# Kernel optimization log

Hardware: AMD Instinct MI355X
Metric: run time of the kernel (lower is better)

The kernel has to match this reference:

```python
import jax, jax.numpy as jnp
import numpy as np

B, V, K = 128, 128000, 20
_SAMPLING_EPS = 1e-5


def setup_inputs() -> dict:
    key = jax.random.key(0)
    k1, k2, k3 = jax.random.split(key, 3)
    logits = jax.random.normal(k1, (B, V), dtype=jnp.float32)
    temp = jax.random.uniform(k2, (B,), dtype=jnp.float32, minval=0.2, maxval=1.5)
    # every 4th sequence is greedy (temperature < eps)
    temp = jnp.where(jnp.arange(B) % 4 == 0, 0.0, temp)
    # uniform noise in (0,1); exponential noise is q = -log(u)
    u = jax.random.uniform(k3, (B, V), dtype=jnp.float32, minval=1e-7, maxval=1.0)
    return {"logits": logits, "temp": temp, "u": u, "max_num_logprobs": K}


def reference(logits, temp, u, max_num_logprobs):
    # apply_temperature: greedy rows (temp < eps) use temp=1.0
    t = jnp.where(temp < _SAMPLING_EPS, 1.0, temp)
    scaled = logits.astype(jnp.float32) / t[:, None]          # [B, V]
    probs = jax.nn.softmax(scaled, axis=-1)                    # [B, V]
    # greedy sample
    greedy = jnp.argmax(probs, axis=1)                         # [B]
    # random sample via exponential-race (Gumbel-max equivalent): argmax(probs / Exp(1))
    q = -jnp.log(u)                                            # Exp(1) noise
    random_sampled = jnp.argmax(probs / q, axis=1)             # [B]
    sampled = jnp.where(temp < _SAMPLING_EPS, greedy, random_sampled)
    # top-k logprobs
    logprobs = jax.nn.log_softmax(scaled, axis=-1)             # [B, V]
    topk_logprobs, topk_indices = jax.lax.top_k(logprobs, max_num_logprobs)
    return sampled, topk_logprobs, topk_indices
```

## Files before the change

kernel.cpp:

```cpp
#include <hip/hip_runtime.h>
#include <stdint.h>


#define KMAX 20
#define SAMPLING_EPS 1e-5f
#define TAU 3.0f
#define CPB 64
#define LOG2E 1.44269504f
#define SMARGIN 3e-4f

static __device__ __forceinline__ float fexp2(float x) {
#if __has_builtin(__builtin_amdgcn_exp2f)
    return __builtin_amdgcn_exp2f(x);
#else
    return exp2f(x);
#endif
}

static __device__ __forceinline__ unsigned int ord32(float v) {
    unsigned int u = __float_as_uint(v);
    return u ^ ((unsigned int)((int)u >> 31) | 0x80000000u);
}
static __device__ __forceinline__ float unord32(unsigned int x) {
    unsigned int u = (x & 0x80000000u) ? (x ^ 0x80000000u) : ~x;
    return __uint_as_float(u);
}
static __device__ __forceinline__ unsigned long long shflxor64(unsigned long long v, int off) {
    int lo = __shfl_xor((int)(unsigned int)v, off, 64);
    int hi = __shfl_xor((int)(unsigned int)(v >> 32), off, 64);
    return ((unsigned long long)(unsigned int)hi << 32) | (unsigned int)lo;
}

static __device__ __forceinline__ float gumbel_exact(float x, float inv_t, float uu, float wm) {
    const float q = (uu > 0.984375f) ? -log1pf(-wm) : -__logf(uu);
    return x * inv_t - __logf(q);
}

static __device__ __forceinline__ float gub_bound(float a, float uu) {
    return fmaf((float)__float_as_uint(1.0f - uu), -0x1p-23f, 127.0f + a);
}

__global__ __launch_bounds__(256, 6) void k1_partials(
        const float* __restrict__ logits, const float* __restrict__ u,
        const float* __restrict__ temp,
        unsigned int* __restrict__ wrec,
        unsigned int* __restrict__ cntbuf,
        uint2* __restrict__ candbuf,
        int V, int nsplit) {
    __shared__ int cnt;
    __shared__ uint2 cand[CPB];
    const int b = blockIdx.x;
    const int t = threadIdx.x;
    const int lane = t & 63;
    const int w = t >> 6;
    if (t == 0) cnt = 0;
    __syncthreads();

    const int nrows = gridDim.x / nsplit;
    const int mb = b % nrows;
    const int sp = b / nrows;
    int r = (mb * 61 + (sp >> 1)) % nrows;
    if ((nrows & (nrows - 1)) == 0) r ^= (r >> 4);
    const int slot = r * nsplit + sp;

    const float traw = temp[r];
    const bool greedy = traw < SAMPLING_EPS;
    const float inv_t = greedy ? 1.0f : (1.0f / traw);
    const float it2 = inv_t * LOG2E;

    const int nf4 = V >> 2;
    const int per = (nf4 + nsplit - 1) / nsplit;
    const int f0 = sp * per;
    const int f1 = min(f0 + per, nf4);

    const float4* __restrict__ l4 = (const float4*)(logits + (size_t)r * V);
    const float4* __restrict__ u4 = (const float4*)(u + (size_t)r * V);

    float s0 = 0.0f, s1 = 0.0f, s2 = 0.0f, s3 = 0.0f;
    float gv = -INFINITY;
    int gcol = 0;

#define PUSH(xv, cc) do { \
        const int pi_ = atomicAdd(&cnt, 1); \
        if (pi_ < CPB) cand[pi_] = make_uint2(__float_as_uint(xv), (unsigned)(cc)); \
    } while (0)

    if (greedy) {
        int f = f0 + t;
        for (; f + 256 < f1; f += 512) {
            const float4 la = l4[f];
            const float4 lb = l4[f + 256];
            s0 += fexp2(la.x * it2); s1 += fexp2(la.y * it2);
            s2 += fexp2(la.z * it2); s3 += fexp2(la.w * it2);
            s0 += fexp2(lb.x * it2); s1 += fexp2(lb.y * it2);
            s2 += fexp2(lb.z * it2); s3 += fexp2(lb.w * it2);
            const float xm = fmaxf(fmaxf(fmaxf(la.x, la.y), fmaxf(la.z, la.w)),
                                   fmaxf(fmaxf(lb.x, lb.y), fmaxf(lb.z, lb.w)));
            if (xm >= TAU) {
                const int c0 = f << 2, c1 = (f + 256) << 2;
                if (la.x >= TAU) PUSH(la.x, c0);
                if (la.y >= TAU) PUSH(la.y, c0 + 1);
                if (la.z >= TAU) PUSH(la.z, c0 + 2);
                if (la.w >= TAU) PUSH(la.w, c0 + 3);
                if (lb.x >= TAU) PUSH(lb.x, c1);
                if (lb.y >= TAU) PUSH(lb.y, c1 + 1);
                if (lb.z >= TAU) PUSH(lb.z, c1 + 2);
                if (lb.w >= TAU) PUSH(lb.w, c1 + 3);
            }
        }
        for (; f < f1; f += 256) {
            const float4 la = l4[f];
            s0 += fexp2(la.x * it2); s1 += fexp2(la.y * it2);
            s2 += fexp2(la.z * it2); s3 += fexp2(la.w * it2);
            const float xm = fmaxf(fmaxf(la.x, la.y), fmaxf(la.z, la.w));
            if (xm >= TAU) {
                const int c0 = f << 2;
                if (la.x >= TAU) PUSH(la.x, c0);
                if (la.y >= TAU) PUSH(la.y, c0 + 1);
                if (la.z >= TAU) PUSH(la.z, c0 + 2);
                if (la.w >= TAU) PUSH(la.w, c0 + 3);
            }
        }
    } else {
        int f = f0 + t;
        if (f < f1) {
            const float4 la = l4[f];
            const float4 ua = u4[f];
            const int c0 = f << 2;
            s0 += fexp2(la.x * it2); s1 += fexp2(la.y * it2);
            s2 += fexp2(la.z * it2); s3 += fexp2(la.w * it2);
            { const float g = gumbel_exact(la.x, inv_t, ua.x, 1.0f - ua.x);
              if (g > gv) { gv = g; gcol = c0; } }
            { const float g = gumbel_exact(la.y, inv_t, ua.y, 1.0f - ua.y);
              if (g > gv) { gv = g; gcol = c0 + 1; } }
            { const float g = gumbel_exact(la.z, inv_t, ua.z, 1.0f - ua.z);
              if (g > gv) { gv = g; gcol = c0 + 2; } }
            { const float g = gumbel_exact(la.w, inv_t, ua.w, 1.0f - ua.w);
              if (g > gv) { gv = g; gcol = c0 + 3; } }
            const float xm = fmaxf(fmaxf(la.x, la.y), fmaxf(la.z, la.w));
            if (xm >= TAU) {
                if (la.x >= TAU) PUSH(la.x, c0);
                if (la.y >= TAU) PUSH(la.y, c0 + 1);
                if (la.z >= TAU) PUSH(la.z, c0 + 2);
                if (la.w >= TAU) PUSH(la.w, c0 + 3);
            }
        }
        float gmax = gv;
        #pragma unroll
        for (int off = 1; off < 64; off <<= 1) gmax = fmaxf(gmax, __shfl_xor(gmax, off, 64));
        float gvs2 = fmaf(gmax, LOG2E, -SMARGIN);

#define EX(gj, xv, uu, cc) \
        if ((gj) > gvs2) { \
            const float wm_ = 1.0f - (uu); \
            const float ge_ = gumbel_exact(xv, inv_t, uu, wm_); \
            if (ge_ > gv) { gv = ge_; gcol = (cc); gvs2 = fmaf(ge_, LOG2E, -SMARGIN); } \
        }

        for (f += 256; f + 256 < f1; f += 512) {
            const float4 la = l4[f];
            const float4 lb = l4[f + 256];
            const float4 ua = u4[f];
            const float4 ub = u4[f + 256];
            const float a0 = la.x * it2, a1 = la.y * it2, a2 = la.z * it2, a3 = la.w * it2;
            const float a4 = lb.x * it2, a5 = lb.y * it2, a6 = lb.z * it2, a7 = lb.w * it2;
            s0 += fexp2(a0); s1 += fexp2(a1); s2 += fexp2(a2); s3 += fexp2(a3);
            s0 += fexp2(a4); s1 += fexp2(a5); s2 += fexp2(a6); s3 += fexp2(a7);
            const float g0 = gub_bound(a0, ua.x), g1 = gub_bound(a1, ua.y);
            const float g2 = gub_bound(a2, ua.z), g3 = gub_bound(a3, ua.w);
            const float g4 = gub_bound(a4, ub.x), g5 = gub_bound(a5, ub.y);
            const float g6 = gub_bound(a6, ub.z), g7 = gub_bound(a7, ub.w);
            const float gm = fmaxf(fmaxf(fmaxf(g0, g1), fmaxf(g2, g3)),
                                   fmaxf(fmaxf(g4, g5), fmaxf(g6, g7)));
            if (gm > gvs2) {
                const int c0 = f << 2, c1 = (f + 256) << 2;
                EX(g0, la.x, ua.x, c0)
                EX(g1, la.y, ua.y, c0 + 1)
                EX(g2, la.z, ua.z, c0 + 2)
                EX(g3, la.w, ua.w, c0 + 3)
                EX(g4, lb.x, ub.x, c1)
                EX(g5, lb.y, ub.y, c1 + 1)
                EX(g6, lb.z, ub.z, c1 + 2)
                EX(g7, lb.w, ub.w, c1 + 3)
            }
            const float xm = fmaxf(fmaxf(fmaxf(la.x, la.y), fmaxf(la.z, la.w)),
                                   fmaxf(fmaxf(lb.x, lb.y), fmaxf(lb.z, lb.w)));
            if (xm >= TAU) {
                const int c0 = f << 2, c1 = (f + 256) << 2;
                if (la.x >= TAU) PUSH(la.x, c0);
                if (la.y >= TAU) PUSH(la.y, c0 + 1);
                if (la.z >= TAU) PUSH(la.z, c0 + 2);
                if (la.w >= TAU) PUSH(la.w, c0 + 3);
                if (lb.x >= TAU) PUSH(lb.x, c1);
                if (lb.y >= TAU) PUSH(lb.y, c1 + 1);
                if (lb.z >= TAU) PUSH(lb.z, c1 + 2);
                if (lb.w >= TAU) PUSH(lb.w, c1 + 3);
            }
        }
        for (; f < f1; f += 256) {
            const float4 la = l4[f];
            const float4 ua = u4[f];
            const float a0 = la.x * it2, a1 = la.y * it2, a2 = la.z * it2, a3 = la.w * it2;
            s0 += fexp2(a0); s1 += fexp2(a1); s2 += fexp2(a2); s3 += fexp2(a3);
            const float g0 = gub_bound(a0, ua.x), g1 = gub_bound(a1, ua.y);
            const float g2 = gub_bound(a2, ua.z), g3 = gub_bound(a3, ua.w);
            const float gm = fmaxf(fmaxf(g0, g1), fmaxf(g2, g3));
            if (gm > gvs2) {
                const int c0 = f << 2;
                EX(g0, la.x, ua.x, c0)
                EX(g1, la.y, ua.y, c0 + 1)
                EX(g2, la.z, ua.z, c0 + 2)
                EX(g3, la.w, ua.w, c0 + 3)
            }
            const float xm = fmaxf(fmaxf(la.x, la.y), fmaxf(la.z, la.w));
            if (xm >= TAU) {
                const int c0 = f << 2;
                if (la.x >= TAU) PUSH(la.x, c0);
                if (la.y >= TAU) PUSH(la.y, c0 + 1);
                if (la.z >= TAU) PUSH(la.z, c0 + 2);
                if (la.w >= TAU) PUSH(la.w, c0 + 3);
            }
        }
#undef EX
    }
#undef PUSH

    float s = (s0 + s1) + (s2 + s3);
    #pragma unroll
    for (int off = 1; off < 64; off <<= 1) s += __shfl_xor(s, off, 64);
    unsigned long long gk = greedy ? 0ull
        : (((unsigned long long)ord32(gv) << 32) | (unsigned int)~(unsigned int)gcol);
    #pragma unroll
    for (int off = 1; off < 64; off <<= 1) {
        const unsigned long long o = shflxor64(gk, off);
        gk = (o > gk) ? o : gk;
    }
    if (lane == 0) {
        unsigned int* rp = wrec + (size_t)(slot * 4 + w) * 4;
        rp[0] = __float_as_uint(s);
        rp[1] = __float_as_uint(unord32((unsigned int)(gk >> 32)));
        rp[2] = ~(unsigned int)gk;
    }
    __syncthreads();
    const int c = cnt;
    if (t == 0) cntbuf[slot] = (unsigned)c;
    if (t < min(c, CPB)) candbuf[(size_t)slot * CPB + t] = cand[t];
}

__global__ __launch_bounds__(64) void k2_finalize(
        const unsigned int* __restrict__ wrec, const unsigned int* __restrict__ cntbuf,
        const uint2* __restrict__ candbuf, const float* __restrict__ logits,
        const float* __restrict__ temp, float* __restrict__ out,
        int B, int V, int K, int nsplit) {
    __shared__ unsigned long long kbuf[512];
    const int r = blockIdx.x;
    const int lane = threadIdx.x;
    const int NW = nsplit * 4;

    const float traw = temp[r];
    const bool greedy = traw < SAMPLING_EPS;
    const float tt = greedy ? 1.0f : traw;

    float s = 0.0f;
    unsigned long long gk = 0ull;
    if (lane < NW) {
        const unsigned int* rp = wrec + (size_t)(r * NW + lane) * 4;
        s = __uint_as_float(rp[0]);
        gk = ((unsigned long long)ord32(__uint_as_float(rp[1])) << 32) | (unsigned int)~rp[2];
    }
    #pragma unroll
    for (int off = 1; off < 64; off <<= 1) s += __shfl_xor(s, off, 64);
    #pragma unroll
    for (int off = 1; off < 64; off <<= 1) {
        const unsigned long long o = shflxor64(gk, off);
        gk = (o > gk) ? o : gk;
    }
    const float lS = logf(s);

    const int cnt_raw = (lane < nsplit) ? (int)cntbuf[r * nsplit + lane] : 0;
    const int cntc = min(cnt_raw, CPB);
    const bool ovf = __ballot(cnt_raw > CPB) != 0ull;
    int incl = cntc;
    #pragma unroll
    for (int d = 1; d < 64; d <<= 1) {
        const int o = __shfl_up(incl, d, 64);
        if (lane >= d) incl += o;
    }
    const int T = __shfl(incl, 63, 64);
    const int off0 = incl - cntc;

    unsigned long long keys[8];
    #pragma unroll
    for (int jj = 0; jj < 8; ++jj) keys[jj] = 0ull;

    if (!ovf && T >= K && T <= 512) {
        if (lane < nsplit) {
            const uint2* cb = candbuf + (size_t)(r * nsplit + lane) * CPB;
            for (int i = 0; i < cntc; ++i) {
                const uint2 e = cb[i];
                kbuf[off0 + i] = ((unsigned long long)ord32(__uint_as_float(e.x)) << 32)
                               | (unsigned int)~e.y;
            }
        }
        __syncthreads();
        #pragma unroll
        for (int jj = 0; jj < 8; ++jj) {
            const int idx = lane + 64 * jj;
            if (idx < T) keys[jj] = kbuf[idx];
        }
    } else {
        unsigned long long mykey = ((unsigned long long)0x007FFFFFu) << 32;
        unsigned long long minkey = mykey;
        float vmin = -INFINITY;
        const float* lr = logits + (size_t)r * V;
        for (int base = 0; base < V; base += 64) {
            const int i = base + lane;
            const float x = (i < V) ? lr[i] : -INFINITY;
            unsigned long long cm = __ballot((i < V) && (x >= vmin));
            while (cm) {
                const int src = (int)__builtin_ctzll(cm);
                cm &= cm - 1;
                const float cv = __shfl(x, src, 64);
                const int cc = __shfl(i, src, 64);
                const unsigned long long ck =
                    ((unsigned long long)ord32(cv) << 32) | (unsigned int)~(unsigned int)cc;
                if (ck > minkey) {
                    const bool own = (lane < K) && (mykey == minkey);
                    const unsigned long long om = __ballot(own);
                    if (lane == (int)__builtin_ctzll(om)) mykey = ck;
                    unsigned long long mk = (lane < K) ? mykey : ~0ull;
                    #pragma unroll
                    for (int o2 = 1; o2 < 64; o2 <<= 1) {
                        const unsigned long long o = shflxor64(mk, o2);
                        mk = (o < mk) ? o : mk;
                    }
                    minkey = mk;
                    vmin = unord32((unsigned int)(mk >> 32));
                }
            }
        }
        keys[0] = (lane < K) ? mykey : 0ull;
    }

    float* out_s  = out;
    float* out_lp = out + B;
    float* out_ix = out + B + (size_t)B * K;

    unsigned int top1 = 0;
    for (int k = 0; k < K; ++k) {
        unsigned long long loc = keys[0];
        #pragma unroll
        for (int jj = 1; jj < 8; ++jj) loc = (keys[jj] > loc) ? keys[jj] : loc;
        #pragma unroll
        for (int off = 1; off < 64; off <<= 1) {
            const unsigned long long o = shflxor64(loc, off);
            loc = (o > loc) ? o : loc;
        }
        #pragma unroll
        for (int jj = 0; jj < 8; ++jj) if (keys[jj] == loc) keys[jj] = 0ull;
        if (lane == 0) {
            const unsigned int col = ~(unsigned int)loc;
            const float v = unord32((unsigned int)(loc >> 32));
            out_lp[(size_t)r * K + k] = v / tt - lS;
            out_ix[(size_t)r * K + k] = (float)col;
            if (k == 0) top1 = col;
        }
    }
    if (lane == 0) {
        out_s[r] = (float)(greedy ? top1 : (~(unsigned int)gk));
    }
}

extern "C" void kernel_launch(void* const* d_in, const int* in_sizes, int n_in,
                              void* d_out, int out_size, void* d_ws, size_t ws_size,
                              hipStream_t stream) {
    const float* logits = (const float*)d_in[0];
    const float* temp   = (const float*)d_in[1];
    const float* u      = (const float*)d_in[2];
    const int B = in_sizes[1];
    const int V = in_sizes[0] / B;
    int K = (out_size - B) / (2 * B);
    if (K > KMAX) K = KMAX;
    if (K < 1) K = 1;

    int nsplit = 16;
    while (nsplit > 1 && (size_t)B * nsplit * 580 > ws_size) nsplit >>= 1;
    const int blocks = B * nsplit;

    unsigned int* wrec   = (unsigned int*)d_ws;
    unsigned int* cntbuf = wrec + (size_t)blocks * 16;
    uint2*        candbf = (uint2*)(cntbuf + blocks);

    k1_partials<<<dim3(blocks), dim3(256), 0, stream>>>(
        logits, u, temp, wrec, cntbuf, candbf, V, nsplit);
    k2_finalize<<<dim3(B), dim3(64), 0, stream>>>(
        wrec, cntbuf, candbf, logits, temp, (float*)d_out, B, V, K, nsplit);
}
```

Baseline: 159.7 us.

## Stage logits and noise through LDS with async global_load_lds double buffering

Replaces the direct register-based float4 streaming loop with a tiled pipeline that copies logits and uniform noise into shared memory using the global_load_lds builtin. It keeps two tiles in flight and syncs twice per tile. Occupancy hint is raised from 6 to 8 waves per SIMD. The aim is to hide memory latency with asynchronous loads. In exchange it adds LDS traffic, two block barriers per 256-element tile, and drops the previous 2x unrolling.

```diff
diff --git a/kernel.cpp b/kernel.cpp
--- a/kernel.cpp
+++ b/kernel.cpp
@@ -8,6 +8,7 @@
 #define CPB 64
 #define LOG2E 1.44269504f
 #define SMARGIN 3e-4f
+#define TILE 256
 
 static __device__ __forceinline__ float fexp2(float x) {
 #if __has_builtin(__builtin_amdgcn_exp2f)
@@ -40,13 +41,25 @@
     return fmaf((float)__float_as_uint(1.0f - uu), -0x1p-23f, 127.0f + a);
 }
 
-__global__ __launch_bounds__(256, 6) void k1_partials(
+static __device__ __forceinline__ void g2lds(const float4* gaddr, float4* lds_wave_base, int lane) {
+#if __has_builtin(__builtin_amdgcn_global_load_lds)
+    __builtin_amdgcn_global_load_lds(
+        (const __attribute__((address_space(1))) void*)gaddr,
+        (__attribute__((address_space(3))) void*)lds_wave_base, 16, 0, 0);
+#else
+    lds_wave_base[lane] = *gaddr;
+#endif
+}
+
+__global__ __launch_bounds__(256, 8) void k1_partials(
         const float* __restrict__ logits, const float* __restrict__ u,
         const float* __restrict__ temp,
         unsigned int* __restrict__ wrec,
         unsigned int* __restrict__ cntbuf,
         uint2* __restrict__ candbuf,
         int V, int nsplit) {
+    __shared__ float4 sL[2][TILE];
+    __shared__ float4 sU[2][TILE];
     __shared__ int cnt;
     __shared__ uint2 cand[CPB];
     const int b = blockIdx.x;
@@ -54,7 +67,6 @@
     const int lane = t & 63;
     const int w = t >> 6;
     if (t == 0) cnt = 0;
-    __syncthreads();
 
     const int nrows = gridDim.x / nsplit;
     const int mb = b % nrows;
@@ -72,6 +84,8 @@
     const int per = (nf4 + nsplit - 1) / nsplit;
     const int f0 = sp * per;
     const int f1 = min(f0 + per, nf4);
+    const int len = f1 - f0;
+    const int ntiles = (len + TILE - 1) / TILE;
 
     const float4* __restrict__ l4 = (const float4*)(logits + (size_t)r * V);
     const float4* __restrict__ u4 = (const float4*)(u + (size_t)r * V);
@@ -79,64 +93,95 @@
     float s0 = 0.0f, s1 = 0.0f, s2 = 0.0f, s3 = 0.0f;
     float gv = -INFINITY;
     int gcol = 0;
+    float gvs2 = INFINITY;
+    const float4 z4 = make_float4(0.f, 0.f, 0.f, 0.f);
+
+#define STAGE(bb, tt) do { \
+        const int si_ = f0 + (tt) * TILE + t; \
+        if (si_ < f1) { \
+            g2lds(l4 + si_, &sL[bb][w * 64], lane); \
+            if (!greedy) g2lds(u4 + si_, &sU[bb][w * 64], lane); \
+        } \
+    } while (0)
 
 #define PUSH(xv, cc) do { \
         const int pi_ = atomicAdd(&cnt, 1); \
         if (pi_ < CPB) cand[pi_] = make_uint2(__float_as_uint(xv), (unsigned)(cc)); \
     } while (0)
 
-    if (greedy) {
-        int f = f0 + t;
-        for (; f + 256 < f1; f += 512) {
-            const float4 la = l4[f];
-            const float4 lb = l4[f + 256];
-            s0 += fexp2(la.x * it2); s1 += fexp2(la.y * it2);
-            s2 += fexp2(la.z * it2); s3 += fexp2(la.w * it2);
-            s0 += fexp2(lb.x * it2); s1 += fexp2(lb.y * it2);
-            s2 += fexp2(lb.z * it2); s3 += fexp2(lb.w * it2);
-            const float xm = fmaxf(fmaxf(fmaxf(la.x, la.y), fmaxf(la.z, la.w)),
-                                   fmaxf(fmaxf(lb.x, lb.y), fmaxf(lb.z, lb.w)));
-            if (xm >= TAU) {
-                const int c0 = f << 2, c1 = (f + 256) << 2;
-                if (la.x >= TAU) PUSH(la.x, c0);
-                if (la.y >= TAU) PUSH(la.y, c0 + 1);
-                if (la.z >= TAU) PUSH(la.z, c0 + 2);
-                if (la.w >= TAU) PUSH(la.w, c0 + 3);
-                if (lb.x >= TAU) PUSH(lb.x, c1);
-                if (lb.y >= TAU) PUSH(lb.y, c1 + 1);
-                if (lb.z >= TAU) PUSH(lb.z, c1 + 2);
-                if (lb.w >= TAU) PUSH(lb.w, c1 + 3);
-            }
-        }
-        for (; f < f1; f += 256) {
-            const float4 la = l4[f];
-            s0 += fexp2(la.x * it2); s1 += fexp2(la.y * it2);
-            s2 += fexp2(la.z * it2); s3 += fexp2(la.w * it2);
-            const float xm = fmaxf(fmaxf(la.x, la.y), fmaxf(la.z, la.w));
-            if (xm >= TAU) {
-                const int c0 = f << 2;
-                if (la.x >= TAU) PUSH(la.x, c0);
-                if (la.y >= TAU) PUSH(la.y, c0 + 1);
-                if (la.z >= TAU) PUSH(la.z, c0 + 2);
-                if (la.w >= TAU) PUSH(la.w, c0 + 3);
-            }
-        }
-    } else {
-        int f = f0 + t;
-        if (f < f1) {
-            const float4 la = l4[f];
-            const float4 ua = u4[f];
-            const int c0 = f << 2;
-            s0 += fexp2(la.x * it2); s1 += fexp2(la.y * it2);
-            s2 += fexp2(la.z * it2); s3 += fexp2(la.w * it2);
-            { const float g = gumbel_exact(la.x, inv_t, ua.x, 1.0f - ua.x);
-              if (g > gv) { gv = g; gcol = c0; } }
-            { const float g = gumbel_exact(la.y, inv_t, ua.y, 1.0f - ua.y);
-              if (g > gv) { gv = g; gcol = c0 + 1; } }
-            { const float g = gumbel_exact(la.z, inv_t, ua.z, 1.0f - ua.z);
-              if (g > gv) { gv = g; gcol = c0 + 2; } }
-            { const float g = gumbel_exact(la.w, inv_t, ua.w, 1.0f - ua.w);
-              if (g > gv) { gv = g; gcol = c0 + 3; } }
+    STAGE(0, 0);
+    if (ntiles > 1) STAGE(1, 1);
+
+    for (int k = 0; k < ntiles; ++k) {
+        __syncthreads();
+        const int idx = f0 + k * TILE + t;
+        const bool act = idx < f1;
+        const int cur = k & 1;
+        float4 la = z4, ua = z4;
+        if (act) {
+            la = sL[cur][t];
+            if (!greedy) ua = sU[cur][t];
+        }
+        __syncthreads();
+        if (k + 2 < ntiles) STAGE(cur, k + 2);
+
+        if (greedy) {
+            if (act) {
+                s0 += fexp2(la.x * it2); s1 += fexp2(la.y * it2);
+                s2 += fexp2(la.z * it2); s3 += fexp2(la.w * it2);
+                const float xm = fmaxf(fmaxf(la.x, la.y), fmaxf(la.z, la.w));
+                if (xm >= TAU) {
+                    const int c0 = idx << 2;
+                    if (la.x >= TAU) PUSH(la.x, c0);
+                    if (la.y >= TAU) PUSH(la.y, c0 + 1);
+                    if (la.z >= TAU) PUSH(la.z, c0 + 2);
+                    if (la.w >= TAU) PUSH(la.w, c0 + 3);
+                }
+            }
+        } else if (k == 0) {
+            if (act) {
+                const int c0 = idx << 2;
+                s0 += fexp2(la.x * it2); s1 += fexp2(la.y * it2);
+                s2 += fexp2(la.z * it2); s3 += fexp2(la.w * it2);
+                { const float g = gumbel_exact(la.x, inv_t, ua.x, 1.0f - ua.x);
+                  if (g > gv) { gv = g; gcol = c0; } }
+                { const float g = gumbel_exact(la.y, inv_t, ua.y, 1.0f - ua.y);
+                  if (g > gv) { gv = g; gcol = c0 + 1; } }
+                { const float g = gumbel_exact(la.z, inv_t, ua.z, 1.0f - ua.z);
+                  if (g > gv) { gv = g; gcol = c0 + 2; } }
+                { const float g = gumbel_exact(la.w, inv_t, ua.w, 1.0f - ua.w);
+                  if (g > gv) { gv = g; gcol = c0 + 3; } }
+                const float xm = fmaxf(fmaxf(la.x, la.y), fmaxf(la.z, la.w));
+                if (xm >= TAU) {
+                    if (la.x >= TAU) PUSH(la.x, c0);
+                    if (la.y >= TAU) PUSH(la.y, c0 + 1);
+                    if (la.z >= TAU) PUSH(la.z, c0 + 2);
+                    if (la.w >= TAU) PUSH(la.w, c0 + 3);
+                }
+            }
+            float gmax = gv;
+            #pragma unroll
+            for (int off = 1; off < 64; off <<= 1) gmax = fmaxf(gmax, __shfl_xor(gmax, off, 64));
+            gvs2 = fmaf(gmax, LOG2E, -SMARGIN);
+        } else if (act) {
+#define EX(gj, xv, uu, cc) \
+            if ((gj) > gvs2) { \
+                const float wm_ = 1.0f - (uu); \
+                const float ge_ = gumbel_exact(xv, inv_t, uu, wm_); \
+                if (ge_ > gv) { gv = ge_; gcol = (cc); gvs2 = fmaf(ge_, LOG2E, -SMARGIN); } \
+            }
+            const int c0 = idx << 2;
+            const float a0 = la.x * it2, a1 = la.y * it2, a2 = la.z * it2, a3 = la.w * it2;
+            s0 += fexp2(a0); s1 += fexp2(a1); s2 += fexp2(a2); s3 += fexp2(a3);
+            const float g0 = gub_bound(a0, ua.x), g1 = gub_bound(a1, ua.y);
+            const float g2 = gub_bound(a2, ua.z), g3 = gub_bound(a3, ua.w);
+            const float gm = fmaxf(fmaxf(g0, g1), fmaxf(g2, g3));
+            if (gm > gvs2) {
+                EX(g0, la.x, ua.x, c0)
+                EX(g1, la.y, ua.y, c0 + 1)
+                EX(g2, la.z, ua.z, c0 + 2)
+                EX(g3, la.w, ua.w, c0 + 3)
+            }
             const float xm = fmaxf(fmaxf(la.x, la.y), fmaxf(la.z, la.w));
             if (xm >= TAU) {
                 if (la.x >= TAU) PUSH(la.x, c0);
@@ -144,86 +189,11 @@
                 if (la.z >= TAU) PUSH(la.z, c0 + 2);
                 if (la.w >= TAU) PUSH(la.w, c0 + 3);
             }
-        }
-        float gmax = gv;
-        #pragma unroll
-        for (int off = 1; off < 64; off <<= 1) gmax = fmaxf(gmax, __shfl_xor(gmax, off, 64));
-        float gvs2 = fmaf(gmax, LOG2E, -SMARGIN);
-
-#define EX(gj, xv, uu, cc) \
-        if ((gj) > gvs2) { \
-            const float wm_ = 1.0f - (uu); \
-            const float ge_ = gumbel_exact(xv, inv_t, uu, wm_); \
-            if (ge_ > gv) { gv = ge_; gcol = (cc); gvs2 = fmaf(ge_, LOG2E, -SMARGIN); } \
-        }
-
-        for (f += 256; f + 256 < f1; f += 512) {
-            const float4 la = l4[f];
-            const float4 lb = l4[f + 256];
-            const float4 ua = u4[f];
-            const float4 ub = u4[f + 256];
-            const float a0 = la.x * it2, a1 = la.y * it2, a2 = la.z * it2, a3 = la.w * it2;
-            const float a4 = lb.x * it2, a5 = lb.y * it2, a6 = lb.z * it2, a7 = lb.w * it2;
-            s0 += fexp2(a0); s1 += fexp2(a1); s2 += fexp2(a2); s3 += fexp2(a3);
-            s0 += fexp2(a4); s1 += fexp2(a5); s2 += fexp2(a6); s3 += fexp2(a7);
-            const float g0 = gub_bound(a0, ua.x), g1 = gub_bound(a1, ua.y);
-            const float g2 = gub_bound(a2, ua.z), g3 = gub_bound(a3, ua.w);
-            const float g4 = gub_bound(a4, ub.x), g5 = gub_bound(a5, ub.y);
-            const float g6 = gub_bound(a6, ub.z), g7 = gub_bound(a7, ub.w);
-            const float gm = fmaxf(fmaxf(fmaxf(g0, g1), fmaxf(g2, g3)),
-                                   fmaxf(fmaxf(g4, g5), fmaxf(g6, g7)));
-            if (gm > gvs2) {
-                const int c0 = f << 2, c1 = (f + 256) << 2;
-                EX(g0, la.x, ua.x, c0)
-                EX(g1, la.y, ua.y, c0 + 1)
-                EX(g2, la.z, ua.z, c0 + 2)
-                EX(g3, la.w, ua.w, c0 + 3)
-                EX(g4, lb.x, ub.x, c1)
-                EX(g5, lb.y, ub.y, c1 + 1)
-                EX(g6, lb.z, ub.z, c1 + 2)
-                EX(g7, lb.w, ub.w, c1 + 3)
-            }
-            const float xm = fmaxf(fmaxf(fmaxf(la.x, la.y), fmaxf(la.z, la.w)),
-                                   fmaxf(fmaxf(lb.x, lb.y), fmaxf(lb.z, lb.w)));
-            if (xm >= TAU) {
-                const int c0 = f << 2, c1 = (f + 256) << 2;
-                if (la.x >= TAU) PUSH(la.x, c0);
-                if (la.y >= TAU) PUSH(la.y, c0 + 1);
-                if (la.z >= TAU) PUSH(la.z, c0 + 2);
-                if (la.w >= TAU) PUSH(la.w, c0 + 3);
-                if (lb.x >= TAU) PUSH(lb.x, c1);
-                if (lb.y >= TAU) PUSH(lb.y, c1 + 1);
-                if (lb.z >= TAU) PUSH(lb.z, c1 + 2);
-                if (lb.w >= TAU) PUSH(lb.w, c1 + 3);
-            }
-        }
-        for (; f < f1; f += 256) {
-            const float4 la = l4[f];
-            const float4 ua = u4[f];
-            const float a0 = la.x * it2, a1 = la.y * it2, a2 = la.z * it2, a3 = la.w * it2;
-            s0 += fexp2(a0); s1 += fexp2(a1); s2 += fexp2(a2); s3 += fexp2(a3);
-            const float g0 = gub_bound(a0, ua.x), g1 = gub_bound(a1, ua.y);
-            const float g2 = gub_bound(a2, ua.z), g3 = gub_bound(a3, ua.w);
-            const float gm = fmaxf(fmaxf(g0, g1), fmaxf(g2, g3));
-            if (gm > gvs2) {
-                const int c0 = f << 2;
-                EX(g0, la.x, ua.x, c0)
-                EX(g1, la.y, ua.y, c0 + 1)
-                EX(g2, la.z, ua.z, c0 + 2)
-                EX(g3, la.w, ua.w, c0 + 3)
-            }
-            const float xm = fmaxf(fmaxf(la.x, la.y), fmaxf(la.z, la.w));
-            if (xm >= TAU) {
-                const int c0 = f << 2;
-                if (la.x >= TAU) PUSH(la.x, c0);
-                if (la.y >= TAU) PUSH(la.y, c0 + 1);
-                if (la.z >= TAU) PUSH(la.z, c0 + 2);
-                if (la.w >= TAU) PUSH(la.w, c0 + 3);
-            }
-        }
 #undef EX
+        }
     }
 #undef PUSH
+#undef STAGE
 
     float s = (s0 + s1) + (s2 + s3);
     #pragma unroll
```

Measured after the change: 163.4 us. 2.3% more time.
